# Kernel optimization log

Hardware: AMD Instinct MI355X
Metric: run time of the kernel (lower is better)

## Reference

```python
import jax, jax.numpy as jnp
import numpy as np

N = 100000      # nodes
E = 1600000     # edges (avg degree 16)
F_IN = 128      # node feature dim
F_E = 8         # edge feature dim
H = 4           # attention heads (layer 1)
C = 16          # hidden per head
T = 1           # target size (layer 2, heads=1, concat=False)
NEG_SLOPE = 0.2


def setup_inputs() -> dict:
    key = jax.random.key(0)
    ks = jax.random.split(key, 20)
    g = lambda k, shape, fan: (jax.random.normal(k, shape, jnp.float32) / np.sqrt(fan))
    return {
        "x": jax.random.normal(ks[0], (N, F_IN), jnp.float32),
        "edge_index": jax.random.randint(ks[1], (2, E), 0, N, dtype=jnp.int32),
        "edge_attr": jax.random.normal(ks[2], (E, F_E), jnp.float32),
        # layer 1 (in=F_IN, out=C, heads=H, concat=True, edge_dim=F_E)
        "Wl1": g(ks[3], (F_IN, H * C), F_IN),
        "bl1": jnp.zeros((H * C,), jnp.float32),
        "Wr1": g(ks[4], (F_IN, H * C), F_IN),
        "br1": jnp.zeros((H * C,), jnp.float32),
        "We1": g(ks[5], (F_E, H * C), F_E),
        "att1": g(ks[6], (H, C), C),
        "b1": jnp.zeros((H * C,), jnp.float32),
        # layer 2 (in=H*C, out=T, heads=1, concat=False, edge_dim=F_E)
        "Wl2": g(ks[7], (H * C, T), H * C),
        "bl2": jnp.zeros((T,), jnp.float32),
        "Wr2": g(ks[8], (H * C, T), H * C),
        "br2": jnp.zeros((T,), jnp.float32),
        "We2": g(ks[9], (F_E, T), F_E),
        "att2": g(ks[10], (1, T), T),
        "b2": jnp.zeros((T,), jnp.float32),
    }


def _gatv2(x, src, dst, eattr, Wl, bl, Wr, br, We, att, bias, heads, out_ch, concat, n_nodes):
    # add self loops, self-loop edge_attr = mean of edge_attr (PyG fill_value='mean')
    loop = jnp.arange(n_nodes, dtype=src.dtype)
    src_a = jnp.concatenate([src, loop])
    dst_a = jnp.concatenate([dst, loop])
    ea = jnp.concatenate(
        [eattr, jnp.broadcast_to(eattr.mean(axis=0), (n_nodes, eattr.shape[1]))], axis=0)

    xl = (x @ Wl + bl).reshape(n_nodes, heads, out_ch)   # source transform
    xr = (x @ Wr + br).reshape(n_nodes, heads, out_ch)   # target transform
    ee = (ea @ We).reshape(-1, heads, out_ch)            # edge transform (no bias)

    # GATv2: score = att . LeakyReLU(x_l[src] + x_r[dst] + W_e e)
    s = jax.nn.leaky_relu(xl[src_a] + xr[dst_a] + ee, NEG_SLOPE)  # [Ea,H,C]
    logits = jnp.einsum('ehc,hc->eh', s, att)                      # [Ea,H]

    # segment softmax over destination nodes (every node has a self loop)
    m = jax.ops.segment_max(logits, dst_a, num_segments=n_nodes)   # [N,H]
    p = jnp.exp(logits - m[dst_a])
    denom = jax.ops.segment_sum(p, dst_a, num_segments=n_nodes)
    alpha = p / denom[dst_a]                                        # [Ea,H]

    out = jax.ops.segment_sum(xl[src_a] * alpha[:, :, None], dst_a,
                              num_segments=n_nodes)                 # [N,H,C]
    out = out.reshape(n_nodes, heads * out_ch) if concat else out.mean(axis=1)
    return out + bias


def reference(x, edge_index, edge_attr, Wl1, bl1, Wr1, br1, We1, att1, b1,
              Wl2, bl2, Wr2, br2, We2, att2, b2):
    src, dst = edge_index[0], edge_index[1]
    # dropout layers are identity at eval time (training=False)
    h = _gatv2(x, src, dst, edge_attr, Wl1, bl1, Wr1, br1, We1, att1, b1,
               H, C, True, N)
    h = jax.nn.elu(h)
    out = _gatv2(h, src, dst, edge_attr, Wl2, bl2, Wr2, br2, We2, att2, b2,
                 1, T, False, N)
    return out
```

## Files before the change

### kernel.cpp

```cpp
#include <hip/hip_runtime.h>
#include <hip/hip_fp16.h>
#include <math.h>

#define N_NODES 100000
#define N_EDGES 1600000
#define N_ITEMS (N_EDGES + N_NODES)
#define F_IN 128
#define HC 64
#define NEG 0.2f
#define SCAN_BS 1024
#define SCAN_NB ((N_NODES + SCAN_BS - 1) / SCAN_BS)
#define MS_BLOCKS 1024

union H2I { __half2 h; int i; };
typedef int v2i __attribute__((ext_vector_type(2)));
typedef int v4i __attribute__((ext_vector_type(4)));

__device__ __forceinline__ __half2 hmax2(__half2 a, __half2 b) {
    H2I ua, ub, uc; ua.h = a; ub.h = b;
    asm("v_pk_max_f16 %0, %1, %2" : "=v"(uc.i) : "v"(ua.i), "v"(ub.i));
    return uc.h;
}

__global__ void mean_sum_kernel(const float* __restrict__ ea, const int* __restrict__ dst,
                                float* __restrict__ partials, unsigned* __restrict__ deg) {
    __shared__ float sh[4][8];
    int stride = gridDim.x * blockDim.x;
    float acc[8] = {0.f,0.f,0.f,0.f,0.f,0.f,0.f,0.f};
    for (int r = blockIdx.x * blockDim.x + threadIdx.x; r < N_EDGES; r += stride) {
        const float4* p = (const float4*)(ea + (size_t)r * 8);
        float4 a = p[0], b = p[1];
        acc[0] += a.x; acc[1] += a.y; acc[2] += a.z; acc[3] += a.w;
        acc[4] += b.x; acc[5] += b.y; acc[6] += b.z; acc[7] += b.w;
        atomicAdd(&deg[dst[r]], 1u);
    }
    int wid  = threadIdx.x >> 6;
    int lane = threadIdx.x & 63;
#pragma unroll
    for (int k = 0; k < 8; k++) {
        float v = acc[k];
        for (int off = 32; off; off >>= 1) v += __shfl_down(v, off);
        if (lane == 0) sh[wid][k] = v;
    }
    __syncthreads();
    if (threadIdx.x < 8) {
        float s = sh[0][threadIdx.x] + sh[1][threadIdx.x] + sh[2][threadIdx.x] + sh[3][threadIdx.x];
        partials[blockIdx.x * 8 + threadIdx.x] = s;
    }
}

__global__ void scan1(const unsigned* __restrict__ deg, unsigned* __restrict__ local_inc,
                      unsigned* __restrict__ bsum,
                      const float* __restrict__ partials, float* __restrict__ sum8) {
    if (blockIdx.x == 0 && threadIdx.x < 64) {
        int lane = threadIdx.x;
        int c = lane & 7, g = lane >> 3;
        float s = 0.f;
        for (int b = g; b < MS_BLOCKS; b += 8) s += partials[b * 8 + c];
        s += __shfl_xor(s, 8);
        s += __shfl_xor(s, 16);
        s += __shfl_xor(s, 32);
        if (lane < 8) sum8[lane] = s;
    }
    __shared__ unsigned wsum[16];
    int i = blockIdx.x * SCAN_BS + threadIdx.x;
    int lane = threadIdx.x & 63;
    int wid  = threadIdx.x >> 6;
    unsigned v = (i < N_NODES) ? (deg[i] + 1u) : 0u;
    unsigned sc = v;
#pragma unroll
    for (int off = 1; off < 64; off <<= 1) {
        unsigned t = __shfl_up(sc, off);
        if (lane >= off) sc += t;
    }
    if (lane == 63) wsum[wid] = sc;
    __syncthreads();
    if (threadIdx.x < 16) {
        unsigned w = wsum[threadIdx.x];
#pragma unroll
        for (int off = 1; off < 16; off <<= 1) {
            unsigned t = __shfl_up(w, off);
            if ((int)threadIdx.x >= off) w += t;
        }
        wsum[threadIdx.x] = w;
    }
    __syncthreads();
    unsigned base = wid ? wsum[wid - 1] : 0u;
    sc += base;
    if (i < N_NODES) local_inc[i] = sc;
    if (threadIdx.x == SCAN_BS - 1) bsum[blockIdx.x] = sc;
}

__global__ void scan23(const unsigned* __restrict__ local_inc, const unsigned* __restrict__ deg,
                       const unsigned* __restrict__ bsum,
                       unsigned* __restrict__ row_start, unsigned* __restrict__ next) {
    __shared__ unsigned tmp[128];
    int t = threadIdx.x;
    if (t < 128) tmp[t] = (t < SCAN_NB) ? bsum[t] : 0u;
    __syncthreads();
    for (int off = 1; off < 128; off <<= 1) {
        unsigned add = 0u;
        if (t < 128 && t >= off) add = tmp[t - off];
        __syncthreads();
        if (t < 128) tmp[t] += add;
        __syncthreads();
    }
    int i = blockIdx.x * blockDim.x + t;
    if (i >= N_NODES) return;
    int b = i >> 10;
    unsigned base = b ? tmp[b - 1] : 0u;
    unsigned v = local_inc[i] - (deg[i] + 1u) + base;
    row_start[i] = v;
    next[i] = v;
}

__global__ void scatter_kernel(const int* __restrict__ src, const int* __restrict__ dst,
                               const float* __restrict__ ea, const float* __restrict__ sum8,
                               const float* __restrict__ We2,
                               unsigned* __restrict__ next,
                               int* __restrict__ rec32) {
    int item = blockIdx.x * blockDim.x + threadIdx.x;
    if (item >= N_ITEMS) return;
    int s, d;
    float4 a, b;
    if (item < N_EDGES) {
        s = src[item]; d = dst[item];
        const float4* p = (const float4*)(ea + (size_t)item * 8);
        a = p[0]; b = p[1];
    } else {
        s = d = item - N_EDGES;
        const float inv = 1.0f / N_EDGES;
        a = make_float4(sum8[0]*inv, sum8[1]*inv, sum8[2]*inv, sum8[3]*inv);
        b = make_float4(sum8[4]*inv, sum8[5]*inv, sum8[6]*inv, sum8[7]*inv);
    }
    float ee2 = a.x*We2[0] + a.y*We2[1] + a.z*We2[2] + a.w*We2[3]
              + b.x*We2[4] + b.y*We2[5] + b.z*We2[6] + b.w*We2[7];
    unsigned pos = atomicAdd(&next[d], 1u);
    H2I e01, e23, e45, e67;
    e01.h = __floats2half2_rn(a.x, a.y);
    e23.h = __floats2half2_rn(a.z, a.w);
    e45.h = __floats2half2_rn(b.x, b.y);
    e67.h = __floats2half2_rn(b.z, b.w);
    int* base = rec32 + (size_t)pos * 8;
    v4i st1; st1.x = s; st1.y = __float_as_int(ee2); st1.z = e01.i; st1.w = e23.i;
    *(v4i*)base = st1;
    v2i st2; st2.x = e45.i; st2.y = e67.i;
    *(v2i*)(base + 4) = st2;
}

__global__ __launch_bounds__(256) void gemm1_kernel(
        const float* __restrict__ x,
        const float* __restrict__ Wl, const float* __restrict__ bl,
        const float* __restrict__ Wr, const float* __restrict__ br,
        __half* __restrict__ xlh, __half* __restrict__ xrh) {
    __shared__ float xs_t[F_IN][36];
    int t = threadIdx.x & 31;
    int g = threadIdx.x >> 5;
    const float* Wsel = (t < 16) ? Wl : Wr;
    const float* bsel = (t < 16) ? bl : br;
    int jc = (t < 16) ? 4 * t : 4 * t - HC;
    float4 bias = *(const float4*)(bsel + jc);
    __half* table = (t < 16) ? xlh : xrh;

    int n0 = blockIdx.x * 32;
    int row = threadIdx.x >> 3;
    int cq  = threadIdx.x & 7;
#pragma unroll
    for (int r = 0; r < 4; r++) {
        int c = cq * 4 + r * 32;
        float4 v = *(const float4*)(x + (size_t)(n0 + row) * F_IN + c);
        xs_t[c + 0][row] = v.x;
        xs_t[c + 1][row] = v.y;
        xs_t[c + 2][row] = v.z;
        xs_t[c + 3][row] = v.w;
    }
    __syncthreads();
    int nb = g * 4;
    float4 a0 = bias, a1 = bias, a2 = bias, a3 = bias;
#pragma unroll 4
    for (int k = 0; k < F_IN; k++) {
        float4 w  = *(const float4*)(Wsel + k * HC + jc);
        float4 xv = *(const float4*)&xs_t[k][nb];
        a0.x += w.x * xv.x; a0.y += w.y * xv.x; a0.z += w.z * xv.x; a0.w += w.w * xv.x;
        a1.x += w.x * xv.y; a1.y += w.y * xv.y; a1.z += w.z * xv.y; a1.w += w.w * xv.y;
        a2.x += w.x * xv.z; a2.y += w.y * xv.z; a2.z += w.z * xv.z; a2.w += w.w * xv.z;
        a3.x += w.x * xv.w; a3.y += w.y * xv.w; a3.z += w.z * xv.w; a3.w += w.w * xv.w;
    }
    float4 arr[4] = {a0, a1, a2, a3};
#pragma unroll
    for (int r = 0; r < 4; r++) {
        H2I u0, u1;
        u0.h = __floats2half2_rn(arr[r].x, arr[r].y);
        u1.h = __floats2half2_rn(arr[r].z, arr[r].w);
        *(int2*)(table + (size_t)(n0 + nb + r) * HC + jc) = make_int2(u0.i, u1.i);
    }
}

__device__ __forceinline__ void edge_update_h(const __half2* __restrict__ weA,
                                              const __half2* __restrict__ weB,
                                              __half2 attA, __half2 attB,
                                              __half2 xr2a, __half2 xr2b,
                                              bool valid, v4i L1, v2i L2, v2i xp,
                                              float& den, float4& acc) {
    H2I ea01, ea23, ea45, ea67, xl01, xl23;
    ea01.i = L1.z; ea23.i = L1.w; ea45.i = L2.x; ea67.i = L2.y;
    xl01.i = xp.x; xl23.i = xp.y;
    __half2 va = __hadd2(xl01.h, xr2a);
    __half2 vb = __hadd2(xl23.h, xr2b);
    __half2 e;
    e = __low2half2(ea01.h);  va = __hfma2(e, weA[0], va); vb = __hfma2(e, weB[0], vb);
    e = __high2half2(ea01.h); va = __hfma2(e, weA[1], va); vb = __hfma2(e, weB[1], vb);
    e = __low2half2(ea23.h);  va = __hfma2(e, weA[2], va); vb = __hfma2(e, weB[2], vb);
    e = __high2half2(ea23.h); va = __hfma2(e, weA[3], va); vb = __hfma2(e, weB[3], vb);
    e = __low2half2(ea45.h);  va = __hfma2(e, weA[4], va); vb = __hfma2(e, weB[4], vb);
    e = __high2half2(ea45.h); va = __hfma2(e, weA[5], va); vb = __hfma2(e, weB[5], vb);
    e = __low2half2(ea67.h);  va = __hfma2(e, weA[6], va); vb = __hfma2(e, weB[6], vb);
    e = __high2half2(ea67.h); va = __hfma2(e, weA[7], va); vb = __hfma2(e, weB[7], vb);
    const __half2 k02 = __float2half2_rn(NEG);
    va = hmax2(va, __hmul2(va, k02));
    vb = hmax2(vb, __hmul2(vb, k02));
    __half2 pd = __hfma2(vb, attB, __hmul2(va, attA));
    float2 pf = __half22float2(pd);
    float prod = pf.x + pf.y;
    prod += __shfl_xor(prod, 1);
    prod += __shfl_xor(prod, 2);
    float p = valid ? __expf(prod) : 0.f;
    float2 xa = __half22float2(xl01.h), xb = __half22float2(xl23.h);
    den   += p;
    acc.x += p * xa.x;
    acc.y += p * xa.y;
    acc.z += p * xb.x;
    acc.w += p * xb.y;
}

__global__ void gat1_kernel(const unsigned* __restrict__ row_start, const unsigned* __restrict__ deg,
                            const int* __restrict__ rec32,
                            const float* __restrict__ We1, const float* __restrict__ att1,
                            const float* __restrict__ b1,
                            const __half* __restrict__ xlh, const __half* __restrict__ xrh,
                            const float* __restrict__ Wl2, const float* __restrict__ bl2,
                            const float* __restrict__ Wr2, const float* __restrict__ br2,
                            float* __restrict__ xl2, float* __restrict__ xr2) {
    int node = blockIdx.x * (blockDim.x >> 6) + (threadIdx.x >> 6);
    int lane = threadIdx.x & 63;
    if (node >= N_NODES) return;
    int g  = lane >> 4;
    int cl = lane & 15;
    unsigned start = row_start[node];
    unsigned cnt   = deg[node] + 1u;
    unsigned cm1   = cnt - 1u;

    __half2 weA[8], weB[8];
#pragma unroll
    for (int k = 0; k < 8; k++) {
        float4 w = *(const float4*)(We1 + k * HC + 4 * cl);
        weA[k] = __floats2half2_rn(w.x, w.y);
        weB[k] = __floats2half2_rn(w.z, w.w);
    }
    float4 at = *(const float4*)(att1 + 4 * cl);
    __half2 attA = __floats2half2_rn(at.x, at.y);
    __half2 attB = __floats2half2_rn(at.z, at.w);
    v2i xrp = *(const v2i*)(xrh + (size_t)node * HC + 4 * cl);
    H2I xru0, xru1; xru0.i = xrp.x; xru1.i = xrp.y;
    __half2 xr2a = xru0.h, xr2b = xru1.h;

    float denA = 0.f, denB = 0.f;
    float4 accA = make_float4(0.f,0.f,0.f,0.f), accB = make_float4(0.f,0.f,0.f,0.f);

#define IDXA(J) (start + min((J) + (unsigned)g, cm1))
#define IDXB(J) (start + min((J) + 4u + (unsigned)g, cm1))
    unsigned iA = IDXA(0u), iB = IDXB(0u);
    v4i L1A = __builtin_nontemporal_load((const v4i*)(rec32 + (size_t)iA * 8));
    v4i L1B = __builtin_nontemporal_load((const v4i*)(rec32 + (size_t)iB * 8));
    v2i L2A = __builtin_nontemporal_load((const v2i*)(rec32 + (size_t)iA * 8 + 4));
    v2i L2B = __builtin_nontemporal_load((const v2i*)(rec32 + (size_t)iB * 8 + 4));
    v2i xpA = *(const v2i*)(xlh + (size_t)L1A.x * HC + 4 * cl);
    v2i xpB = *(const v2i*)(xlh + (size_t)L1B.x * HC + 4 * cl);

    for (unsigned j = 0; j < cnt; j += 8) {
        v4i c1A = L1A, c1B = L1B;
        v2i c2A = L2A, c2B = L2B, cxA = xpA, cxB = xpB;
        bool vA = (j + g) < cnt, vB = (j + 4 + g) < cnt;
        if (j + 8 < cnt) {
            iA = IDXA(j + 8); iB = IDXB(j + 8);
            L1A = __builtin_nontemporal_load((const v4i*)(rec32 + (size_t)iA * 8));
            L1B = __builtin_nontemporal_load((const v4i*)(rec32 + (size_t)iB * 8));
            L2A = __builtin_nontemporal_load((const v2i*)(rec32 + (size_t)iA * 8 + 4));
            L2B = __builtin_nontemporal_load((const v2i*)(rec32 + (size_t)iB * 8 + 4));
            xpA = *(const v2i*)(xlh + (size_t)L1A.x * HC + 4 * cl);
            xpB = *(const v2i*)(xlh + (size_t)L1B.x * HC + 4 * cl);
        }
        edge_update_h(weA, weB, attA, attB, xr2a, xr2b, vA, c1A, c2A, cxA, denA, accA);
        edge_update_h(weA, weB, attA, attB, xr2a, xr2b, vB, c1B, c2B, cxB, denB, accB);
    }
#undef IDXA
#undef IDXB

    float den = denA + denB;
    float4 acc;
    acc.x = accA.x + accB.x;
    acc.y = accA.y + accB.y;
    acc.z = accA.z + accB.z;
    acc.w = accA.w + accB.w;

    den   += __shfl_xor(den, 16);   den   += __shfl_xor(den, 32);
    acc.x += __shfl_xor(acc.x, 16); acc.x += __shfl_xor(acc.x, 32);
    acc.y += __shfl_xor(acc.y, 16); acc.y += __shfl_xor(acc.y, 32);
    acc.z += __shfl_xor(acc.z, 16); acc.z += __shfl_xor(acc.z, 32);
    acc.w += __shfl_xor(acc.w, 16); acc.w += __shfl_xor(acc.w, 32);

    float4 b1v  = *(const float4*)(b1 + 4 * cl);
    float4 wl2v = *(const float4*)(Wl2 + 4 * cl);
    float4 wr2v = *(const float4*)(Wr2 + 4 * cl);
    float inv_den = 1.f / den;
    float4 o;
    o.x = acc.x * inv_den + b1v.x;
    o.y = acc.y * inv_den + b1v.y;
    o.z = acc.z * inv_den + b1v.z;
    o.w = acc.w * inv_den + b1v.w;
    o.x = o.x > 0.f ? o.x : __expf(o.x) - 1.f;
    o.y = o.y > 0.f ? o.y : __expf(o.y) - 1.f;
    o.z = o.z > 0.f ? o.z : __expf(o.z) - 1.f;
    o.w = o.w > 0.f ? o.w : __expf(o.w) - 1.f;
    float sl = o.x*wl2v.x + o.y*wl2v.y + o.z*wl2v.z + o.w*wl2v.w;
    float sr = o.x*wr2v.x + o.y*wr2v.y + o.z*wr2v.z + o.w*wr2v.w;
#pragma unroll
    for (int off = 1; off <= 8; off <<= 1) {
        sl += __shfl_xor(sl, off);
        sr += __shfl_xor(sr, off);
    }
    if (lane == 0) {
        xl2[node] = sl + bl2[0];
        xr2[node] = sr + br2[0];
    }
}

__global__ __launch_bounds__(256) void gat2_kernel(
        const unsigned* __restrict__ row_start, const unsigned* __restrict__ deg,
        const int* __restrict__ rec32, const float* __restrict__ att2,
        const float* __restrict__ xl2, const float* __restrict__ xr2,
        const float* __restrict__ b2, float* __restrict__ out) {
    int wave = threadIdx.x >> 6;
    int lane = threadIdx.x & 63;
    int sub  = lane >> 4;
    int l    = lane & 15;
    int node = (blockIdx.x * 4 + wave) * 4 + sub;
    unsigned start = row_start[node];
    unsigned cnt   = deg[node] + 1u;
    float xrv = xr2[node];
    float a2  = att2[0];
    float den = 0.f, num = 0.f;
    for (unsigned idx = (unsigned)l; idx < cnt; idx += 16) {
        v2i r = __builtin_nontemporal_load((const v2i*)(rec32 + (size_t)(start + idx) * 8));
        float ee = __int_as_float(r.y);
        float xv = xl2[r.x];
        float v = xv + xrv + ee;
        v = fmaxf(v, NEG * v);
        float p = __expf(a2 * v);
        den += p;
        num += p * xv;
    }
#pragma unroll
    for (int off = 1; off <= 8; off <<= 1) {
        den += __shfl_xor(den, off);
        num += __shfl_xor(num, off);
    }
    if (l == 0) out[node] = num / den + b2[0];
}

extern "C" void kernel_launch(void* const* d_in, const int* in_sizes, int n_in,
                              void* d_out, int out_size, void* d_ws, size_t ws_size,
                              hipStream_t stream) {
    const float* x    = (const float*)d_in[0];
    const int*   ei   = (const int*)d_in[1];
    const float* ea   = (const float*)d_in[2];
    const float* Wl1  = (const float*)d_in[3];
    const float* bl1  = (const float*)d_in[4];
    const float* Wr1  = (const float*)d_in[5];
    const float* br1  = (const float*)d_in[6];
    const float* We1  = (const float*)d_in[7];
    const float* att1 = (const float*)d_in[8];
    const float* b1   = (const float*)d_in[9];
    const float* Wl2  = (const float*)d_in[10];
    const float* bl2  = (const float*)d_in[11];
    const float* Wr2  = (const float*)d_in[12];
    const float* br2  = (const float*)d_in[13];
    const float* We2  = (const float*)d_in[14];
    const float* att2 = (const float*)d_in[15];
    const float* b2   = (const float*)d_in[16];

    const int* src = ei;
    const int* dst = ei + N_EDGES;

    float* W = (float*)d_ws;
    size_t o = 0;
    float*    sum8      = W + o;               o += 8;
    float*    partials  = W + o;               o += MS_BLOCKS * 8;
    unsigned* deg       = (unsigned*)(W + o);  o += N_NODES;
    unsigned* local_inc = (unsigned*)(W + o);  o += N_NODES;
    unsigned* bsum      = (unsigned*)(W + o);  o += 128;
    unsigned* row_start = (unsigned*)(W + o);  o += N_NODES;
    unsigned* next      = (unsigned*)(W + o);  o += N_NODES;
    o = (o + 7) & ~(size_t)7;
    int*      rec32     = (int*)(W + o);       o += (size_t)N_ITEMS * 8;
    __half*   xlh       = (__half*)(W + o);    o += (size_t)N_NODES * (HC/2);
    __half*   xrh       = (__half*)(W + o);    o += (size_t)N_NODES * (HC/2);
    float*    xl2       = W + o;               o += N_NODES;
    float*    xr2       = W + o;               o += N_NODES;

    hipMemsetAsync(deg, 0, (size_t)N_NODES * sizeof(unsigned), stream);
    mean_sum_kernel<<<MS_BLOCKS, 256, 0, stream>>>(ea, dst, partials, deg);
    scan1<<<SCAN_NB, SCAN_BS, 0, stream>>>(deg, local_inc, bsum, partials, sum8);
    scan23<<<(N_NODES + 255) / 256, 256, 0, stream>>>(local_inc, deg, bsum, row_start, next);
    scatter_kernel<<<(N_ITEMS + 255) / 256, 256, 0, stream>>>(
        src, dst, ea, sum8, We2, next, rec32);
    gemm1_kernel<<<N_NODES / 32, 256, 0, stream>>>(x, Wl1, bl1, Wr1, br1, xlh, xrh);
    gat1_kernel<<<(N_NODES + 3) / 4, 256, 0, stream>>>(
        row_start, deg, rec32, We1, att1, b1, xlh, xrh,
        Wl2, bl2, Wr2, br2, xl2, xr2);
    gat2_kernel<<<N_NODES / 16, 256, 0, stream>>>(
        row_start, deg, rec32, att2, xl2, xr2, b2, (float*)d_out);
}
```

Measured before the change: 405.8 us.

## Use fp16 dot2 GEMM with LDS-staged weights and pack row start/count

The layer-1 feature GEMM is rewritten to stage both weight matrices into LDS as packed fp16 pairs along K. The x tile is also converted to fp16 pairs, and the inner loop uses v_dot2 instructions (fp16 products, fp32 accumulate) in place of scalar fp32 FMAs with global weight loads. Separately, row_start and deg+1 are packed into one uint2 array so the gather kernels fetch both with a single load. This cuts ALU and global-load work in the GEMM, at the cost of fp16 rounding on inputs and weights, extra LDS use and a per-block weight conversion.

```diff
diff --git a/kernel.cpp b/kernel.cpp
--- a/kernel.cpp
+++ b/kernel.cpp
@@ -15,6 +15,17 @@
 union H2I { __half2 h; int i; };
 typedef int v2i __attribute__((ext_vector_type(2)));
 typedef int v4i __attribute__((ext_vector_type(4)));
+typedef _Float16 h2 __attribute__((ext_vector_type(2)));
+
+#if __has_builtin(__builtin_amdgcn_fdot2)
+__device__ __forceinline__ float DOT2(h2 a, h2 b, float c) {
+    return __builtin_amdgcn_fdot2(a, b, c, false);
+}
+#else
+__device__ __forceinline__ float DOT2(h2 a, h2 b, float c) {
+    return c + (float)a.x * (float)b.x + (float)a.y * (float)b.y;
+}
+#endif
 
 __device__ __forceinline__ __half2 hmax2(__half2 a, __half2 b) {
     H2I ua, ub, uc; ua.h = a; ub.h = b;
@@ -93,7 +104,7 @@
 
 __global__ void scan23(const unsigned* __restrict__ local_inc, const unsigned* __restrict__ deg,
                        const unsigned* __restrict__ bsum,
-                       unsigned* __restrict__ row_start, unsigned* __restrict__ next) {
+                       unsigned* __restrict__ next, uint2* __restrict__ row_info) {
     __shared__ unsigned tmp[128];
     int t = threadIdx.x;
     if (t < 128) tmp[t] = (t < SCAN_NB) ? bsum[t] : 0u;
@@ -109,9 +120,10 @@
     if (i >= N_NODES) return;
     int b = i >> 10;
     unsigned base = b ? tmp[b - 1] : 0u;
-    unsigned v = local_inc[i] - (deg[i] + 1u) + base;
-    row_start[i] = v;
+    unsigned cnt = deg[i] + 1u;
+    unsigned v = local_inc[i] - cnt + base;
     next[i] = v;
+    row_info[i] = make_uint2(v, cnt);
 }
 
 __global__ void scatter_kernel(const int* __restrict__ src, const int* __restrict__ dst,
@@ -153,38 +165,57 @@
         const float* __restrict__ Wl, const float* __restrict__ bl,
         const float* __restrict__ Wr, const float* __restrict__ br,
         __half* __restrict__ xlh, __half* __restrict__ xrh) {
-    __shared__ float xs_t[F_IN][36];
+    __shared__ h2 W16[64][128];
+    __shared__ h2 xs16[64][36];
     int t = threadIdx.x & 31;
     int g = threadIdx.x >> 5;
-    const float* Wsel = (t < 16) ? Wl : Wr;
+    int n0 = blockIdx.x * 32;
+
+    for (int i = threadIdx.x; i < 64 * 16; i += 256) {
+        int kk = i >> 4, cq = i & 15;
+        float4 w0 = *(const float4*)(Wl + (size_t)(2*kk)   * HC + 4*cq);
+        float4 w1 = *(const float4*)(Wl + (size_t)(2*kk+1) * HC + 4*cq);
+        h2 p;
+        p.x = (_Float16)w0.x; p.y = (_Float16)w1.x; W16[kk][4*cq+0] = p;
+        p.x = (_Float16)w0.y; p.y = (_Float16)w1.y; W16[kk][4*cq+1] = p;
+        p.x = (_Float16)w0.z; p.y = (_Float16)w1.z; W16[kk][4*cq+2] = p;
+        p.x = (_Float16)w0.w; p.y = (_Float16)w1.w; W16[kk][4*cq+3] = p;
+        float4 v0 = *(const float4*)(Wr + (size_t)(2*kk)   * HC + 4*cq);
+        float4 v1 = *(const float4*)(Wr + (size_t)(2*kk+1) * HC + 4*cq);
+        p.x = (_Float16)v0.x; p.y = (_Float16)v1.x; W16[kk][64+4*cq+0] = p;
+        p.x = (_Float16)v0.y; p.y = (_Float16)v1.y; W16[kk][64+4*cq+1] = p;
+        p.x = (_Float16)v0.z; p.y = (_Float16)v1.z; W16[kk][64+4*cq+2] = p;
+        p.x = (_Float16)v0.w; p.y = (_Float16)v1.w; W16[kk][64+4*cq+3] = p;
+    }
+    {
+        int row = threadIdx.x >> 3;
+        int cq  = threadIdx.x & 7;
+#pragma unroll
+        for (int r = 0; r < 4; r++) {
+            int c = cq * 4 + r * 32;
+            float4 v = *(const float4*)(x + (size_t)(n0 + row) * F_IN + c);
+            h2 p;
+            p.x = (_Float16)v.x; p.y = (_Float16)v.y; xs16[c/2][row]     = p;
+            p.x = (_Float16)v.z; p.y = (_Float16)v.w; xs16[c/2 + 1][row] = p;
+        }
+    }
+    __syncthreads();
+
     const float* bsel = (t < 16) ? bl : br;
     int jc = (t < 16) ? 4 * t : 4 * t - HC;
     float4 bias = *(const float4*)(bsel + jc);
     __half* table = (t < 16) ? xlh : xrh;
-
-    int n0 = blockIdx.x * 32;
-    int row = threadIdx.x >> 3;
-    int cq  = threadIdx.x & 7;
-#pragma unroll
-    for (int r = 0; r < 4; r++) {
-        int c = cq * 4 + r * 32;
-        float4 v = *(const float4*)(x + (size_t)(n0 + row) * F_IN + c);
-        xs_t[c + 0][row] = v.x;
-        xs_t[c + 1][row] = v.y;
-        xs_t[c + 2][row] = v.z;
-        xs_t[c + 3][row] = v.w;
-    }
-    __syncthreads();
     int nb = g * 4;
+
     float4 a0 = bias, a1 = bias, a2 = bias, a3 = bias;
 #pragma unroll 4
-    for (int k = 0; k < F_IN; k++) {
-        float4 w  = *(const float4*)(Wsel + k * HC + jc);
-        float4 xv = *(const float4*)&xs_t[k][nb];
-        a0.x += w.x * xv.x; a0.y += w.y * xv.x; a0.z += w.z * xv.x; a0.w += w.w * xv.x;
-        a1.x += w.x * xv.y; a1.y += w.y * xv.y; a1.z += w.z * xv.y; a1.w += w.w * xv.y;
-        a2.x += w.x * xv.z; a2.y += w.y * xv.z; a2.z += w.z * xv.z; a2.w += w.w * xv.z;
-        a3.x += w.x * xv.w; a3.y += w.y * xv.w; a3.z += w.z * xv.w; a3.w += w.w * xv.w;
+    for (int kk = 0; kk < 64; kk++) {
+        h2 w0 = W16[kk][4*t+0], w1 = W16[kk][4*t+1], w2 = W16[kk][4*t+2], w3 = W16[kk][4*t+3];
+        h2 x0 = xs16[kk][nb+0], x1 = xs16[kk][nb+1], x2 = xs16[kk][nb+2], x3 = xs16[kk][nb+3];
+        a0.x = DOT2(x0, w0, a0.x); a0.y = DOT2(x0, w1, a0.y); a0.z = DOT2(x0, w2, a0.z); a0.w = DOT2(x0, w3, a0.w);
+        a1.x = DOT2(x1, w0, a1.x); a1.y = DOT2(x1, w1, a1.y); a1.z = DOT2(x1, w2, a1.z); a1.w = DOT2(x1, w3, a1.w);
+        a2.x = DOT2(x2, w0, a2.x); a2.y = DOT2(x2, w1, a2.y); a2.z = DOT2(x2, w2, a2.z); a2.w = DOT2(x2, w3, a2.w);
+        a3.x = DOT2(x3, w0, a3.x); a3.y = DOT2(x3, w1, a3.y); a3.z = DOT2(x3, w2, a3.z); a3.w = DOT2(x3, w3, a3.w);
     }
     float4 arr[4] = {a0, a1, a2, a3};
 #pragma unroll
@@ -233,7 +264,7 @@
     acc.w += p * xb.y;
 }
 
-__global__ void gat1_kernel(const unsigned* __restrict__ row_start, const unsigned* __restrict__ deg,
+__global__ void gat1_kernel(const uint2* __restrict__ row_info,
                             const int* __restrict__ rec32,
                             const float* __restrict__ We1, const float* __restrict__ att1,
                             const float* __restrict__ b1,
@@ -246,8 +277,9 @@
     if (node >= N_NODES) return;
     int g  = lane >> 4;
     int cl = lane & 15;
-    unsigned start = row_start[node];
-    unsigned cnt   = deg[node] + 1u;
+    uint2 ri = row_info[node];
+    unsigned start = ri.x;
+    unsigned cnt   = ri.y;
     unsigned cm1   = cnt - 1u;
 
     __half2 weA[8], weB[8];
@@ -336,7 +368,7 @@
 }
 
 __global__ __launch_bounds__(256) void gat2_kernel(
-        const unsigned* __restrict__ row_start, const unsigned* __restrict__ deg,
+        const uint2* __restrict__ row_info,
         const int* __restrict__ rec32, const float* __restrict__ att2,
         const float* __restrict__ xl2, const float* __restrict__ xr2,
         const float* __restrict__ b2, float* __restrict__ out) {
@@ -345,8 +377,9 @@
     int sub  = lane >> 4;
     int l    = lane & 15;
     int node = (blockIdx.x * 4 + wave) * 4 + sub;
-    unsigned start = row_start[node];
-    unsigned cnt   = deg[node] + 1u;
+    uint2 ri = row_info[node];
+    unsigned start = ri.x;
+    unsigned cnt   = ri.y;
     float xrv = xr2[node];
     float a2  = att2[0];
     float den = 0.f, num = 0.f;
@@ -399,8 +432,8 @@
     unsigned* deg       = (unsigned*)(W + o);  o += N_NODES;
     unsigned* local_inc = (unsigned*)(W + o);  o += N_NODES;
     unsigned* bsum      = (unsigned*)(W + o);  o += 128;
-    unsigned* row_start = (unsigned*)(W + o);  o += N_NODES;
     unsigned* next      = (unsigned*)(W + o);  o += N_NODES;
+    uint2*    row_info  = (uint2*)(W + o);     o += (size_t)N_NODES * 2;
     o = (o + 7) & ~(size_t)7;
     int*      rec32     = (int*)(W + o);       o += (size_t)N_ITEMS * 8;
     __half*   xlh       = (__half*)(W + o);    o += (size_t)N_NODES * (HC/2);
@@ -411,13 +444,13 @@
     hipMemsetAsync(deg, 0, (size_t)N_NODES * sizeof(unsigned), stream);
     mean_sum_kernel<<<MS_BLOCKS, 256, 0, stream>>>(ea, dst, partials, deg);
     scan1<<<SCAN_NB, SCAN_BS, 0, stream>>>(deg, local_inc, bsum, partials, sum8);
-    scan23<<<(N_NODES + 255) / 256, 256, 0, stream>>>(local_inc, deg, bsum, row_start, next);
+    scan23<<<(N_NODES + 255) / 256, 256, 0, stream>>>(local_inc, deg, bsum, next, row_info);
     scatter_kernel<<<(N_ITEMS + 255) / 256, 256, 0, stream>>>(
         src, dst, ea, sum8, We2, next, rec32);
     gemm1_kernel<<<N_NODES / 32, 256, 0, stream>>>(x, Wl1, bl1, Wr1, br1, xlh, xrh);
     gat1_kernel<<<(N_NODES + 3) / 4, 256, 0, stream>>>(
-        row_start, deg, rec32, We1, att1, b1, xlh, xrh,
+        row_info, rec32, We1, att1, b1, xlh, xrh,
         Wl2, bl2, Wr2, br2, xl2, xr2);
     gat2_kernel<<<N_NODES / 16, 256, 0, stream>>>(
-        row_start, deg, rec32, att2, xl2, xr2, b2, (float*)d_out);
-}
+        row_info, rec32, att2, xl2, xr2, b2, (float*)d_out);
+}
```

After: 392.3 us, median of 2. 1.03x faster.
